# Performance work log

Measured on AMD Instinct MI355X. Metric: run time of the kernel, lower is better.

The kernel has to match this reference:

```python
import jax, jax.numpy as jnp
import numpy as np

B, C, T = 8, 512, 1024
EXP = 2
E = EXP * C          # 1024, gate/value width
H, HD = 8, 64        # heads, qk head dim
QK = H * HD          # 512
AVG_LEN = 512
EPS = 1e-5


def setup_inputs() -> dict:
    key = jax.random.key(0)
    ks = jax.random.split(key, 10)
    s = 0.02
    return {
        "x": jax.random.normal(ks[0], (B, C, T), jnp.float32),
        "W_in": jax.random.normal(ks[1], (2 * E, C), jnp.float32) * s,
        "b_in": jnp.zeros((2 * E,), jnp.float32),
        "W_attn": jax.random.normal(ks[2], (QK, C), jnp.float32) * s,
        "b_attn": jnp.zeros((QK,), jnp.float32),
        "w_q": 1.0 + jax.random.normal(ks[3], (QK,), jnp.float32) * 0.1,
        "b_q": jax.random.normal(ks[4], (QK,), jnp.float32) * 0.1,
        "w_k": 1.0 + jax.random.normal(ks[5], (QK,), jnp.float32) * 0.1,
        "b_k": jax.random.normal(ks[6], (QK,), jnp.float32) * 0.1,
        "W_out": jax.random.normal(ks[7], (C, E), jnp.float32) * s,
        "b_out": jnp.zeros((C,), jnp.float32),
        "gamma": jnp.ones((C,), jnp.float32),
    }


def reference(x, W_in, b_in, W_attn, b_attn, w_q, b_q, w_k, b_k, W_out, b_out, gamma):
    residual = x
    # mlp_in (1x1 conv) + SiLU, then chunk into gate u and value v, each (B,E,T)
    uv = jax.nn.silu(jnp.einsum('oc,bct->bot', W_in, x) + b_in[:, None])
    u, v = uv[:, :E], uv[:, E:]
    # mlp_attn (1x1 conv); no activation (activation_attn unused in forward)
    z = jnp.einsum('oc,bct->bot', W_attn, x) + b_attn[:, None]  # (B,QK,T)
    # depthwise 1x1 conv on cat(z,z) = two independent per-channel affines
    q = z * w_q[:, None] + b_q[:, None]
    k = z * w_k[:, None] + b_k[:, None]
    # split heads: q,k -> (B,H,T,HD); v -> (B,H,T,E//H)
    q = q.reshape(B, H, HD, T).transpose(0, 1, 3, 2)
    k = k.reshape(B, H, HD, T).transpose(0, 1, 3, 2)
    vh = v.reshape(B, H, E // H, T).transpose(0, 1, 3, 2)
    # entropy-invariant scale: (log n / log avg_len) / sqrt(d)
    scale = (np.log(T) / np.log(AVG_LEN)) / np.sqrt(HD)
    scores = jnp.einsum('bhqd,bhkd->bhqk', q, k) * jnp.float32(scale)
    attn = jax.nn.softmax(scores, axis=-1)
    o = jnp.einsum('bhqk,bhke->bhqe', attn, vh)        # (B,H,T,E//H)
    o = o.transpose(0, 1, 3, 2).reshape(B, E, T)       # back to (B,E,T)
    # gate, project out, residual + RMSNorm over channel dim
    out = jnp.einsum('ce,bet->bct', W_out, u * o) + b_out[:, None]
    y = residual + out
    rms = jax.lax.rsqrt(jnp.mean(y * y, axis=1, keepdims=True) + EPS)
    return y * rms * gamma[:, None]
```

## Files before the change

kernel.cpp:

```cpp
#include <hip/hip_runtime.h>

typedef __attribute__((ext_vector_type(8))) short short8;
typedef __attribute__((ext_vector_type(4))) float f32x4;
typedef __attribute__((ext_vector_type(16))) float f32x16;

__device__ __forceinline__ unsigned short f2b(float f) {
  union { float f; unsigned u; } x; x.f = f;
  unsigned r = (x.u + 0x7fffu + ((x.u >> 16) & 1u)) >> 16;
  return (unsigned short)r;
}
__device__ __forceinline__ float b2f(unsigned short b) {
  union { unsigned u; float f; } x; x.u = ((unsigned)b) << 16;
  return x.f;
}
__device__ __forceinline__ unsigned cvtpk(float lo, float hi) {
  unsigned r;
  asm("v_cvt_pk_bf16_f32 %0, %1, %2" : "=v"(r) : "v"(lo), "v"(hi));
  return r;
}
__device__ __forceinline__ void plswap(unsigned& a, unsigned& b) {
  asm volatile("v_permlane32_swap_b32 %0, %1" : "+v"(a), "+v"(b));
}

#define GLDS16(gp, lp)                                                                  \
  __builtin_amdgcn_global_load_lds((const __attribute__((address_space(1))) void*)(gp), \
                                   (__attribute__((address_space(3))) void*)(lp), 16, 0, 0)

__global__ void prep_w_kernel(const float* __restrict__ W_in, const float* __restrict__ W_attn,
                              const float* __restrict__ W_out, unsigned short* __restrict__ Wcat,
                              unsigned short* __restrict__ WoutB) {
  const int n1 = 2048 * 512, n2 = 512 * 512, n3 = 512 * 1024;
  for (int i = blockIdx.x * 256 + threadIdx.x; i < n1 + n2 + n3; i += gridDim.x * 256) {
    if (i < n1) Wcat[i] = f2b(W_in[i]);
    else if (i < n1 + n2) Wcat[i] = f2b(W_attn[i - n1]);
    else WoutB[i - n1 - n2] = f2b(W_out[i - n1 - n2]);
  }
}

__global__ __launch_bounds__(256) void transpose_x_kernel(const float* __restrict__ x,
                                                          unsigned short* __restrict__ xT) {
  __shared__ float tile[32][33];
  const int bid = blockIdx.x;
  const int b = bid >> 9;
  const int rem = bid & 511;
  const int c0 = (rem >> 5) << 5;
  const int t0 = (rem & 31) << 5;
  const int tj = threadIdx.x & 31, ti = threadIdx.x >> 5;
#pragma unroll
  for (int r = 0; r < 32; r += 8)
    tile[ti + r][tj] = x[(((size_t)b << 9) + c0 + ti + r) * 1024 + t0 + tj];
  __syncthreads();
#pragma unroll
  for (int r = 0; r < 32; r += 8)
    xT[(((size_t)b << 10) + t0 + ti + r) * 512 + c0 + tj] = f2b(tile[tj][ti + r]);
}

__device__ __forceinline__ void gemm_stage(const unsigned short* Ag, const unsigned short* Bg,
                                           int lda, int ldb, int k0, unsigned short* lsA,
                                           unsigned short* lsB, int buf, int sr, int sk,
                                           int ldst) {
  const int bb = buf * 8192;
  GLDS16(Ag + (size_t)sr * lda + k0 + sk, (char*)lsA + bb + ldst);
  GLDS16(Ag + (size_t)(sr + 64) * lda + k0 + sk, (char*)lsA + bb + 4096 + ldst);
  GLDS16(Bg + (size_t)sr * ldb + k0 + sk, (char*)lsB + bb + ldst);
  GLDS16(Bg + (size_t)(sr + 64) * ldb + k0 + sk, (char*)lsB + bb + 4096 + ldst);
}

__device__ __forceinline__ void gemm_bt_core(const unsigned short* __restrict__ Ag,
                                             const unsigned short* __restrict__ Bg, int lda,
                                             int ldb, int K, unsigned short* lsA,
                                             unsigned short* lsB, f32x4 acc[4][4]) {
  const int tid = threadIdx.x;
  const int lane = tid & 63;
  const int w = tid >> 6;
  const int wr = w >> 1, wc = w & 1;
  const int sr = tid >> 2;
  const int sk = (tid & 3) << 3;
  const int ldst = (tid >> 6) << 10;

  const int nt = K >> 5;
  gemm_stage(Ag, Bg, lda, ldb, 0, lsA, lsB, 0, sr, sk, ldst);
  for (int t = 0; t < nt; ++t) {
    const int cur = t & 1;
    if (t + 1 < nt) {
      gemm_stage(Ag, Bg, lda, ldb, (t + 1) << 5, lsA, lsB, cur ^ 1, sr, sk, ldst);
      asm volatile("s_waitcnt vmcnt(4)" ::: "memory");
    } else {
      asm volatile("s_waitcnt vmcnt(0)" ::: "memory");
    }
    __builtin_amdgcn_s_barrier();
    short8 af[4], bfr[4];
    const int bb = cur * 8192;
    const int ko = (lane >> 4) << 4;
    const int ra = (wr << 6) + (lane & 15);
    const int rb = (wc << 6) + (lane & 15);
#pragma unroll
    for (int mi = 0; mi < 4; ++mi)
      af[mi] = *(const short8*)((const char*)lsA + bb + ((ra + (mi << 4)) << 6) + ko);
#pragma unroll
    for (int ni = 0; ni < 4; ++ni)
      bfr[ni] = *(const short8*)((const char*)lsB + bb + ((rb + (ni << 4)) << 6) + ko);
#pragma unroll
    for (int mi = 0; mi < 4; ++mi)
#pragma unroll
      for (int ni = 0; ni < 4; ++ni)
        acc[mi][ni] =
            __builtin_amdgcn_mfma_f32_16x16x32_bf16(af[mi], bfr[ni], acc[mi][ni], 0, 0, 0);
    __builtin_amdgcn_s_barrier();
  }
}

__global__ __launch_bounds__(256) void gemm_a_kernel(
    const unsigned short* __restrict__ Wcat, const unsigned short* __restrict__ xT,
    const float* __restrict__ b_in, const float* __restrict__ b_attn,
    const float* __restrict__ w_q, const float* __restrict__ b_q, const float* __restrict__ w_k,
    const float* __restrict__ b_k, unsigned short* __restrict__ u, unsigned short* __restrict__ v,
    unsigned short* __restrict__ qT, unsigned short* __restrict__ kT) {
  __shared__ __align__(16) unsigned short lsA[8192];
  __shared__ __align__(16) unsigned short lsB[8192];
  const int bid = ((blockIdx.x & 7) * 160) + (blockIdx.x >> 3);
  const int b = bid / 160;
  const int rem = bid % 160;
  const int m0 = (rem >> 3) << 7;
  const int n0 = (rem & 7) << 7;
  f32x4 acc[4][4];
  const f32x4 z4 = {0.f, 0.f, 0.f, 0.f};
#pragma unroll
  for (int mi = 0; mi < 4; ++mi)
#pragma unroll
    for (int ni = 0; ni < 4; ++ni) acc[mi][ni] = z4;

  const unsigned short* Ag = Wcat + (size_t)m0 * 512;
  const unsigned short* Bg = xT + ((size_t)b << 19) + ((size_t)n0 << 9);
  gemm_bt_core(Ag, Bg, 512, 512, 512, lsA, lsB, acc);

  const int lane = threadIdx.x & 63;
  const int w = threadIdx.x >> 6;
  const int wr = w >> 1, wc = w & 1;
#pragma unroll
  for (int mi = 0; mi < 4; ++mi) {
    const int row0 = m0 + (wr << 6) + (mi << 4) + ((lane >> 4) << 2);
#pragma unroll
    for (int ni = 0; ni < 4; ++ni) {
      const int col = n0 + (wc << 6) + (ni << 4) + (lane & 15);
      if (row0 < 2048) {
#pragma unroll
        for (int i = 0; i < 4; ++i) {
          const int row = row0 + i;
          const float s = acc[mi][ni][i] + b_in[row];
          const float r = s / (1.f + __expf(-s));
          if (row < 1024)
            u[((((size_t)b << 10) + row) << 10) + col] = f2b(r);
          else
            v[((((size_t)b << 10) + (row - 1024)) << 10) + col] = f2b(r);
        }
      } else {
        const int c0 = row0 - 2048;
        ushort4 qv, kv;
        unsigned short* qp = (unsigned short*)&qv;
        unsigned short* kp = (unsigned short*)&kv;
#pragma unroll
        for (int i = 0; i < 4; ++i) {
          const int c = c0 + i;
          const float z = acc[mi][ni][i] + b_attn[c];
          qp[i] = f2b(z * w_q[c] + b_q[c]);
          kp[i] = f2b(z * w_k[c] + b_k[c]);
        }
        const int h = c0 >> 6, d = c0 & 63;
        const size_t base = ((((size_t)b * 8 + h) << 10) + col) * 64 + d;
        *(ushort4*)(qT + base) = qv;
        *(ushort4*)(kT + base) = kv;
      }
    }
  }
}

__global__ __launch_bounds__(256, 3) void attn_kernel(const unsigned short* __restrict__ qT,
                                                      const unsigned short* __restrict__ kT,
                                                      const unsigned short* __restrict__ v,
                                                      const unsigned short* __restrict__ u,
                                                      unsigned short* __restrict__ uoT) {
  __shared__ __align__(16) unsigned short Kls[2][4096];
  __shared__ __align__(16) unsigned short Vls[2][8192];
  __shared__ float lsumP[2][64];
  const float SCALE = 0.13888888888888889f;
  const int bid = blockIdx.x;
  const int bh = bid & 63;
  const int qb = bid >> 6;
  const int b = bh >> 3, h = bh & 7;
  const int tid = threadIdx.x;
  const int lane = tid & 63;
  const int w = tid >> 6;
  const int l5 = lane >> 5;
  const int l31 = lane & 31;
  const int qw = w >> 1, kw = w & 1;
  const int q0 = qb << 6;

  const unsigned short* qh = qT + ((size_t)bh << 16);
  const unsigned short* kh = kT + ((size_t)bh << 16);
  const unsigned short* vh = v + ((((size_t)b << 10) + (h << 7)) << 10);

  short8 qf[4];
#pragma unroll
  for (int ds = 0; ds < 4; ++ds)
    qf[ds] = *(const short8*)(qh + (size_t)(q0 + (qw << 5) + l31) * 64 + (ds << 4) + (l5 << 3));

  f32x16 o[4];
#pragma unroll
  for (int eb = 0; eb < 4; ++eb)
#pragma unroll
    for (int i = 0; i < 16; ++i) o[eb][i] = 0.f;
  float lacc = 0.f;

  const int srow = lane >> 3;
  const int scol = (((lane & 7) ^ srow) << 3);

#define ATTN_STAGE(buf, kt)                                                  \
  {                                                                          \
    const int t2 = (kt) << 6;                                                \
    _Pragma("unroll") for (int j = 0; j < 2; ++j)                            \
        GLDS16(kh + (size_t)(t2 + (w << 4) + (j << 3) + srow) * 64 + scol,   \
               (char*)Kls[buf] + (w << 11) + (j << 10));                     \
    _Pragma("unroll") for (int j = 0; j < 4; ++j)                            \
        GLDS16(vh + (size_t)((w << 5) + (j << 3) + srow) * 1024 + t2 + scol, \
               (char*)Vls[buf] + (w << 12) + (j << 10));                     \
  }

  ATTN_STAGE(0, 0);
  const int krow = (kw << 5) + l31;
  for (int kt = 0; kt < 16; ++kt) {
    const int cur = kt & 1;
    if (kt < 15) {
      ATTN_STAGE(cur ^ 1, kt + 1);
      asm volatile("s_waitcnt vmcnt(6)" ::: "memory");
    } else {
      asm volatile("s_waitcnt vmcnt(0)" ::: "memory");
    }
    __builtin_amdgcn_s_barrier();

    f32x16 s;
#pragma unroll
    for (int i = 0; i < 16; ++i) s[i] = 0.f;
    const char* kbase = (const char*)Kls[cur];
#pragma unroll
    for (int ds = 0; ds < 4; ++ds) {
      short8 kf = *(const short8*)(kbase + (krow << 7) +
                                   (((ds << 5) + (l5 << 4)) ^ ((krow & 7) << 4)));
      s = __builtin_amdgcn_mfma_f32_32x32x16_bf16(kf, qf[ds], s, 0, 0, 0);
    }
    float p[16];
#pragma unroll
    for (int i = 0; i < 16; ++i) {
      p[i] = __expf(s[i] * SCALE);
      lacc += p[i];
    }
    unsigned W00 = cvtpk(p[0], p[1]), W01 = cvtpk(p[2], p[3]);
    unsigned W10 = cvtpk(p[4], p[5]), W11 = cvtpk(p[6], p[7]);
    unsigned W20 = cvtpk(p[8], p[9]), W21 = cvtpk(p[10], p[11]);
    unsigned W30 = cvtpk(p[12], p[13]), W31 = cvtpk(p[14], p[15]);
    union { short8 s8; unsigned u4[4]; } pf0, pf1;
    {
      unsigned a = W10, bq = W00; plswap(a, bq);
      pf0.u4[0] = bq; pf0.u4[2] = a;
      unsigned c = W11, d = W01; plswap(c, d);
      pf0.u4[1] = d; pf0.u4[3] = c;
      unsigned e = W30, f = W20; plswap(e, f);
      pf1.u4[0] = f; pf1.u4[2] = e;
      unsigned g = W31, hh = W21; plswap(g, hh);
      pf1.u4[1] = hh; pf1.u4[3] = g;
    }

    const char* vbase = (const char*)Vls[cur];
#pragma unroll
    for (int eb = 0; eb < 4; ++eb) {
      const int vrow = (eb << 5) + l31;
      short8 vf0 = *(const short8*)(vbase + (vrow << 7) +
                                    ((((kw << 6)) + (l5 << 4)) ^ ((vrow & 7) << 4)));
      o[eb] = __builtin_amdgcn_mfma_f32_32x32x16_bf16(vf0, pf0.s8, o[eb], 0, 0, 0);
      short8 vf1 = *(const short8*)(vbase + (vrow << 7) +
                                    ((((kw << 6) + 32) + (l5 << 4)) ^ ((vrow & 7) << 4)));
      o[eb] = __builtin_amdgcn_mfma_f32_32x32x16_bf16(vf1, pf1.s8, o[eb], 0, 0, 0);
    }
    __builtin_amdgcn_s_barrier();
  }
#undef ATTN_STAGE

  lacc += __shfl_xor(lacc, 32, 64);
  if (l5 == 0) lsumP[kw][(qw << 5) + l31] = lacc;
  __syncthreads();

  float* red = (float*)Vls;
  if (kw == 1) {
#pragma unroll
    for (int eb = 0; eb < 4; ++eb)
#pragma unroll
      for (int i = 0; i < 16; ++i)
        red[((((qw << 2) + eb) << 10)) + (i << 6) + lane] = o[eb][i];
  }
  __syncthreads();

  if (kw == 0) {
    const int q = (qw << 5) + l31;
    const float rl = 1.f / (lsumP[0][q] + lsumP[1][q]);
    const int t = q0 + q;
#pragma unroll
    for (int eb = 0; eb < 4; ++eb) {
#pragma unroll
      for (int a = 0; a < 4; ++a) {
        const int e4 = (eb << 5) + (a << 3) + (l5 << 2);
        const int eg = (h << 7) + e4;
        ushort4 outv;
        unsigned short* op = (unsigned short*)&outv;
#pragma unroll
        for (int j = 0; j < 4; ++j) {
          const int i = (a << 2) + j;
          const float oo =
              (o[eb][i] + red[((((qw << 2) + eb) << 10)) + (i << 6) + lane]) * rl;
          const float uu = b2f(u[((((size_t)b << 10) + eg + j) << 10) + t]);
          op[j] = f2b(oo * uu);
        }
        *(ushort4*)(uoT + ((((size_t)b << 10) + t) << 10) + eg) = outv;
      }
    }
  }
}

__global__ __launch_bounds__(256) void gemm_c_kernel(const unsigned short* __restrict__ uoT,
                                                     const unsigned short* __restrict__ WoutB,
                                                     const float* __restrict__ x,
                                                     const float* __restrict__ b_out,
                                                     float* __restrict__ y) {
  __shared__ __align__(16) unsigned short lsA[8192];
  __shared__ __align__(16) unsigned short lsB[8192];
  const int bid = ((blockIdx.x & 7) * 32) + (blockIdx.x >> 3);
  const int b = bid >> 5;
  const int rem = bid & 31;
  const int m0 = (rem >> 2) << 7;
  const int n0 = (rem & 3) << 7;
  f32x4 acc[4][4];
  const f32x4 z4 = {0.f, 0.f, 0.f, 0.f};
#pragma unroll
  for (int mi = 0; mi < 4; ++mi)
#pragma unroll
    for (int ni = 0; ni < 4; ++ni) acc[mi][ni] = z4;

  const unsigned short* Ag = uoT + ((size_t)b << 20) + ((size_t)m0 << 10);
  const unsigned short* Bg = WoutB + ((size_t)n0 << 10);
  gemm_bt_core(Ag, Bg, 1024, 1024, 1024, lsA, lsB, acc);

  const int lane = threadIdx.x & 63;
  const int w = threadIdx.x >> 6;
  const int wr = w >> 1, wc = w & 1;
#pragma unroll
  for (int mi = 0; mi < 4; ++mi) {
    const int t4 = m0 + (wr << 6) + (mi << 4) + ((lane >> 4) << 2);
#pragma unroll
    for (int ni = 0; ni < 4; ++ni) {
      const int c = n0 + (wc << 6) + (ni << 4) + (lane & 15);
      const size_t base = ((((size_t)b << 9) + c) << 10) + t4;
      const f32x4 xv = *(const f32x4*)(x + base);
      const float bo = b_out[c];
      f32x4 o;
#pragma unroll
      for (int i = 0; i < 4; ++i) o[i] = acc[mi][ni][i] + bo + xv[i];
      *(f32x4*)(y + base) = o;
    }
  }
}

__global__ __launch_bounds__(256) void rms_kernel(const float* __restrict__ y,
                                                  const float* __restrict__ gamma,
                                                  float* __restrict__ out) {
  __shared__ float part[16][16];
  __shared__ float rmsv[16];
  const int bid = blockIdx.x;
  const int b = bid >> 6;
  const int t0 = (bid & 63) << 4;
  const int tid = threadIdx.x;
  const int tc = tid & 15, cg = tid >> 4;
  const int t = t0 + tc;
  float ss = 0.f;
  for (int c = cg * 32; c < cg * 32 + 32; ++c) {
    const float vv = y[((((size_t)b << 9) + c) << 10) + t];
    ss += vv * vv;
  }
  part[cg][tc] = ss;
  __syncthreads();
  if (tid < 16) {
    float tot = 0.f;
#pragma unroll
    for (int g = 0; g < 16; ++g) tot += part[g][tid];
    rmsv[tid] = rsqrtf(tot / 512.f + 1e-5f);
  }
  __syncthreads();
  const float rm = rmsv[tc];
  for (int c = cg * 32; c < cg * 32 + 32; ++c) {
    const size_t o = ((((size_t)b << 9) + c) << 10) + t;
    out[o] = y[o] * rm * gamma[c];
  }
}

extern "C" void kernel_launch(void* const* d_in, const int* in_sizes, int n_in, void* d_out,
                              int out_size, void* d_ws, size_t ws_size, hipStream_t stream) {
  const float* x = (const float*)d_in[0];
  const float* W_in = (const float*)d_in[1];
  const float* b_in = (const float*)d_in[2];
  const float* W_attn = (const float*)d_in[3];
  const float* b_attn = (const float*)d_in[4];
  const float* w_q = (const float*)d_in[5];
  const float* b_q = (const float*)d_in[6];
  const float* w_k = (const float*)d_in[7];
  const float* b_k = (const float*)d_in[8];
  const float* W_out = (const float*)d_in[9];
  const float* b_out = (const float*)d_in[10];
  const float* gamma = (const float*)d_in[11];
  float* out = (float*)d_out;

  char* ws = (char*)d_ws;
  size_t off = 0;
  auto alloc = [&](size_t bytes) {
    char* p = ws + off;
    off += (bytes + 255) & ~(size_t)255;
    return p;
  };
  unsigned short* Wcat = (unsigned short*)alloc((size_t)2560 * 512 * 2);
  unsigned short* WoutB = (unsigned short*)alloc((size_t)512 * 1024 * 2);
  unsigned short* xT = (unsigned short*)alloc((size_t)8 * 1024 * 512 * 2);
  unsigned short* u = (unsigned short*)alloc((size_t)8 * 1024 * 1024 * 2);
  unsigned short* v = (unsigned short*)alloc((size_t)8 * 1024 * 1024 * 2);
  unsigned short* qT = (unsigned short*)alloc((size_t)8 * 8 * 1024 * 64 * 2);
  unsigned short* kT = (unsigned short*)alloc((size_t)8 * 8 * 1024 * 64 * 2);
  unsigned short* uoT = (unsigned short*)alloc((size_t)8 * 1024 * 1024 * 2);
  float* y = (float*)alloc((size_t)8 * 512 * 1024 * 4);
  if (off > ws_size) return;

  prep_w_kernel<<<896, 256, 0, stream>>>(W_in, W_attn, W_out, Wcat, WoutB);
  transpose_x_kernel<<<4096, 256, 0, stream>>>(x, xT);
  gemm_a_kernel<<<1280, 256, 0, stream>>>(Wcat, xT, b_in, b_attn, w_q, b_q, w_k, b_k, u, v, qT,
                                          kT);
  attn_kernel<<<1024, 256, 0, stream>>>(qT, kT, v, u, uoT);
  gemm_c_kernel<<<256, 256, 0, stream>>>(uoT, WoutB, x, b_out, y);
  rms_kernel<<<512, 256, 0, stream>>>(y, gamma, out);
}
```

Measured before the change: 141.9 us.

## Restructure attention to split value columns per wave, remove cross-wave reduction

The attention kernel now uses 512-thread blocks over 128 queries. Each wave computes all 64 keys of a tile for its 32 queries and accumulates half of the 128 value columns, so the shared-memory reduction of partial outputs and row sums is no longer needed. It also adds XCD-aware block mapping and s_setprio around the MFMA sections. Separately, the RMS kernel keeps y values in registers to avoid re-reading them, and the GEMM kernels double their static LDS arrays, which may lower occupancy.

```diff
diff --git a/kernel.cpp b/kernel.cpp
--- a/kernel.cpp
+++ b/kernel.cpp
@@ -116,8 +116,8 @@
     const float* __restrict__ w_q, const float* __restrict__ b_q, const float* __restrict__ w_k,
     const float* __restrict__ b_k, unsigned short* __restrict__ u, unsigned short* __restrict__ v,
     unsigned short* __restrict__ qT, unsigned short* __restrict__ kT) {
-  __shared__ __align__(16) unsigned short lsA[8192];
-  __shared__ __align__(16) unsigned short lsB[8192];
+  __shared__ __align__(16) unsigned short lsA[16384];
+  __shared__ __align__(16) unsigned short lsB[16384];
   const int bid = ((blockIdx.x & 7) * 160) + (blockIdx.x >> 3);
   const int b = bid / 160;
   const int rem = bid % 160;
@@ -175,26 +175,26 @@
   }
 }
 
-__global__ __launch_bounds__(256, 3) void attn_kernel(const unsigned short* __restrict__ qT,
+__global__ __launch_bounds__(512, 4) void attn_kernel(const unsigned short* __restrict__ qT,
                                                       const unsigned short* __restrict__ kT,
                                                       const unsigned short* __restrict__ v,
                                                       const unsigned short* __restrict__ u,
                                                       unsigned short* __restrict__ uoT) {
   __shared__ __align__(16) unsigned short Kls[2][4096];
   __shared__ __align__(16) unsigned short Vls[2][8192];
-  __shared__ float lsumP[2][64];
   const float SCALE = 0.13888888888888889f;
-  const int bid = blockIdx.x;
-  const int bh = bid & 63;
-  const int qb = bid >> 6;
+  const int bx = blockIdx.x;
+  const int xcd = bx & 7, idx = bx >> 3;
+  const int bh = (xcd << 3) + (idx & 7);
+  const int qb = idx >> 3;
   const int b = bh >> 3, h = bh & 7;
   const int tid = threadIdx.x;
   const int lane = tid & 63;
   const int w = tid >> 6;
   const int l5 = lane >> 5;
   const int l31 = lane & 31;
-  const int qw = w >> 1, kw = w & 1;
-  const int q0 = qb << 6;
+  const int qw = w >> 1, eh = w & 1;
+  const int q0 = qb << 7;
 
   const unsigned short* qh = qT + ((size_t)bh << 16);
   const unsigned short* kh = kT + ((size_t)bh << 16);
@@ -205,122 +205,142 @@
   for (int ds = 0; ds < 4; ++ds)
     qf[ds] = *(const short8*)(qh + (size_t)(q0 + (qw << 5) + l31) * 64 + (ds << 4) + (l5 << 3));
 
-  f32x16 o[4];
-#pragma unroll
-  for (int eb = 0; eb < 4; ++eb)
+  f32x16 o[2];
+#pragma unroll
+  for (int eb = 0; eb < 2; ++eb)
 #pragma unroll
     for (int i = 0; i < 16; ++i) o[eb][i] = 0.f;
   float lacc = 0.f;
 
-  const int srow = lane >> 3;
-  const int scol = (((lane & 7) ^ srow) << 3);
-
-#define ATTN_STAGE(buf, kt)                                                  \
-  {                                                                          \
-    const int t2 = (kt) << 6;                                                \
-    _Pragma("unroll") for (int j = 0; j < 2; ++j)                            \
-        GLDS16(kh + (size_t)(t2 + (w << 4) + (j << 3) + srow) * 64 + scol,   \
-               (char*)Kls[buf] + (w << 11) + (j << 10));                     \
-    _Pragma("unroll") for (int j = 0; j < 4; ++j)                            \
-        GLDS16(vh + (size_t)((w << 5) + (j << 3) + srow) * 1024 + t2 + scol, \
-               (char*)Vls[buf] + (w << 12) + (j << 10));                     \
+  const int srow = tid >> 3;
+  const int scol = (((tid & 7) ^ (srow & 7)) << 3);
+
+#define ATTN_STAGE(buf, kt)                                                        \
+  {                                                                                \
+    const int t2 = (kt) << 6;                                                      \
+    GLDS16(kh + (size_t)(t2 + srow) * 64 + scol, (char*)Kls[buf] + (w << 10));     \
+    GLDS16(vh + ((size_t)srow << 10) + t2 + scol, (char*)Vls[buf] + (w << 10));    \
+    GLDS16(vh + ((size_t)(64 + srow) << 10) + t2 + scol,                           \
+           (char*)Vls[buf] + 8192 + (w << 10));                                    \
   }
 
   ATTN_STAGE(0, 0);
-  const int krow = (kw << 5) + l31;
+  union U8 { short8 s8; unsigned u4[4]; };
   for (int kt = 0; kt < 16; ++kt) {
     const int cur = kt & 1;
     if (kt < 15) {
       ATTN_STAGE(cur ^ 1, kt + 1);
-      asm volatile("s_waitcnt vmcnt(6)" ::: "memory");
+      asm volatile("s_waitcnt vmcnt(3)" ::: "memory");
     } else {
       asm volatile("s_waitcnt vmcnt(0)" ::: "memory");
     }
     __builtin_amdgcn_s_barrier();
 
-    f32x16 s;
-#pragma unroll
-    for (int i = 0; i < 16; ++i) s[i] = 0.f;
-    const char* kbase = (const char*)Kls[cur];
-#pragma unroll
-    for (int ds = 0; ds < 4; ++ds) {
-      short8 kf = *(const short8*)(kbase + (krow << 7) +
-                                   (((ds << 5) + (l5 << 4)) ^ ((krow & 7) << 4)));
-      s = __builtin_amdgcn_mfma_f32_32x32x16_bf16(kf, qf[ds], s, 0, 0, 0);
-    }
-    float p[16];
-#pragma unroll
-    for (int i = 0; i < 16; ++i) {
-      p[i] = __expf(s[i] * SCALE);
-      lacc += p[i];
-    }
-    unsigned W00 = cvtpk(p[0], p[1]), W01 = cvtpk(p[2], p[3]);
-    unsigned W10 = cvtpk(p[4], p[5]), W11 = cvtpk(p[6], p[7]);
-    unsigned W20 = cvtpk(p[8], p[9]), W21 = cvtpk(p[10], p[11]);
-    unsigned W30 = cvtpk(p[12], p[13]), W31 = cvtpk(p[14], p[15]);
-    union { short8 s8; unsigned u4[4]; } pf0, pf1;
+    const char* kb = (const char*)Kls[cur];
+    const char* vb = (const char*)Vls[cur];
+    U8 pf[4];
+
     {
+      f32x16 s;
+#pragma unroll
+      for (int i = 0; i < 16; ++i) s[i] = 0.f;
+      const int kr = l31;
+      __builtin_amdgcn_s_setprio(1);
+#pragma unroll
+      for (int ds = 0; ds < 4; ++ds) {
+        short8 kf = *(const short8*)(kb + (kr << 7) +
+                                     (((ds << 5) + (l5 << 4)) ^ ((kr & 7) << 4)));
+        s = __builtin_amdgcn_mfma_f32_32x32x16_bf16(kf, qf[ds], s, 0, 0, 0);
+      }
+      __builtin_amdgcn_s_setprio(0);
+      float p[16];
+#pragma unroll
+      for (int i = 0; i < 16; ++i) {
+        p[i] = __expf(s[i] * SCALE);
+        lacc += p[i];
+      }
+      unsigned W00 = cvtpk(p[0], p[1]), W01 = cvtpk(p[2], p[3]);
+      unsigned W10 = cvtpk(p[4], p[5]), W11 = cvtpk(p[6], p[7]);
+      unsigned W20 = cvtpk(p[8], p[9]), W21 = cvtpk(p[10], p[11]);
+      unsigned W30 = cvtpk(p[12], p[13]), W31 = cvtpk(p[14], p[15]);
       unsigned a = W10, bq = W00; plswap(a, bq);
-      pf0.u4[0] = bq; pf0.u4[2] = a;
+      pf[0].u4[0] = bq; pf[0].u4[2] = a;
       unsigned c = W11, d = W01; plswap(c, d);
-      pf0.u4[1] = d; pf0.u4[3] = c;
+      pf[0].u4[1] = d; pf[0].u4[3] = c;
       unsigned e = W30, f = W20; plswap(e, f);
-      pf1.u4[0] = f; pf1.u4[2] = e;
+      pf[1].u4[0] = f; pf[1].u4[2] = e;
       unsigned g = W31, hh = W21; plswap(g, hh);
-      pf1.u4[1] = hh; pf1.u4[3] = g;
-    }
-
-    const char* vbase = (const char*)Vls[cur];
-#pragma unroll
-    for (int eb = 0; eb < 4; ++eb) {
-      const int vrow = (eb << 5) + l31;
-      short8 vf0 = *(const short8*)(vbase + (vrow << 7) +
-                                    ((((kw << 6)) + (l5 << 4)) ^ ((vrow & 7) << 4)));
-      o[eb] = __builtin_amdgcn_mfma_f32_32x32x16_bf16(vf0, pf0.s8, o[eb], 0, 0, 0);
-      short8 vf1 = *(const short8*)(vbase + (vrow << 7) +
-                                    ((((kw << 6) + 32) + (l5 << 4)) ^ ((vrow & 7) << 4)));
-      o[eb] = __builtin_amdgcn_mfma_f32_32x32x16_bf16(vf1, pf1.s8, o[eb], 0, 0, 0);
-    }
+      pf[1].u4[1] = hh; pf[1].u4[3] = g;
+    }
+    {
+      f32x16 s;
+#pragma unroll
+      for (int i = 0; i < 16; ++i) s[i] = 0.f;
+      const int kr = 32 + l31;
+      __builtin_amdgcn_s_setprio(1);
+#pragma unroll
+      for (int ds = 0; ds < 4; ++ds) {
+        short8 kf = *(const short8*)(kb + (kr << 7) +
+                                     (((ds << 5) + (l5 << 4)) ^ ((kr & 7) << 4)));
+        s = __builtin_amdgcn_mfma_f32_32x32x16_bf16(kf, qf[ds], s, 0, 0, 0);
+      }
+      __builtin_amdgcn_s_setprio(0);
+      float p[16];
+#pragma unroll
+      for (int i = 0; i < 16; ++i) {
+        p[i] = __expf(s[i] * SCALE);
+        lacc += p[i];
+      }
+      unsigned W00 = cvtpk(p[0], p[1]), W01 = cvtpk(p[2], p[3]);
+      unsigned W10 = cvtpk(p[4], p[5]), W11 = cvtpk(p[6], p[7]);
+      unsigned W20 = cvtpk(p[8], p[9]), W21 = cvtpk(p[10], p[11]);
+      unsigned W30 = cvtpk(p[12], p[13]), W31 = cvtpk(p[14], p[15]);
+      unsigned a = W10, bq = W00; plswap(a, bq);
+      pf[2].u4[0] = bq; pf[2].u4[2] = a;
+      unsigned c = W11, d = W01; plswap(c, d);
+      pf[2].u4[1] = d; pf[2].u4[3] = c;
+      unsigned e = W30, f = W20; plswap(e, f);
+      pf[3].u4[0] = f; pf[3].u4[2] = e;
+      unsigned g = W31, hh = W21; plswap(g, hh);
+      pf[3].u4[1] = hh; pf[3].u4[3] = g;
+    }
+
+    __builtin_amdgcn_s_setprio(1);
+#pragma unroll
+    for (int eb = 0; eb < 2; ++eb) {
+      const int vrow = (eh << 6) + (eb << 5) + l31;
+#pragma unroll
+      for (int ks = 0; ks < 4; ++ks) {
+        short8 vf = *(const short8*)(vb + (vrow << 7) +
+                                     (((ks << 5) + (l5 << 4)) ^ ((vrow & 7) << 4)));
+        o[eb] = __builtin_amdgcn_mfma_f32_32x32x16_bf16(vf, pf[ks].s8, o[eb], 0, 0, 0);
+      }
+    }
+    __builtin_amdgcn_s_setprio(0);
     __builtin_amdgcn_s_barrier();
   }
 #undef ATTN_STAGE
 
   lacc += __shfl_xor(lacc, 32, 64);
-  if (l5 == 0) lsumP[kw][(qw << 5) + l31] = lacc;
-  __syncthreads();
-
-  float* red = (float*)Vls;
-  if (kw == 1) {
-#pragma unroll
-    for (int eb = 0; eb < 4; ++eb)
-#pragma unroll
-      for (int i = 0; i < 16; ++i)
-        red[((((qw << 2) + eb) << 10)) + (i << 6) + lane] = o[eb][i];
-  }
-  __syncthreads();
-
-  if (kw == 0) {
-    const int q = (qw << 5) + l31;
-    const float rl = 1.f / (lsumP[0][q] + lsumP[1][q]);
-    const int t = q0 + q;
-#pragma unroll
-    for (int eb = 0; eb < 4; ++eb) {
-#pragma unroll
-      for (int a = 0; a < 4; ++a) {
-        const int e4 = (eb << 5) + (a << 3) + (l5 << 2);
-        const int eg = (h << 7) + e4;
-        ushort4 outv;
-        unsigned short* op = (unsigned short*)&outv;
-#pragma unroll
-        for (int j = 0; j < 4; ++j) {
-          const int i = (a << 2) + j;
-          const float oo =
-              (o[eb][i] + red[((((qw << 2) + eb) << 10)) + (i << 6) + lane]) * rl;
-          const float uu = b2f(u[((((size_t)b << 10) + eg + j) << 10) + t]);
-          op[j] = f2b(oo * uu);
-        }
-        *(ushort4*)(uoT + ((((size_t)b << 10) + t) << 10) + eg) = outv;
-      }
+  const float rl = 1.f / lacc;
+  const int t = q0 + (qw << 5) + l31;
+
+#pragma unroll
+  for (int eb = 0; eb < 2; ++eb) {
+#pragma unroll
+    for (int a = 0; a < 4; ++a) {
+      const int e4 = (eh << 6) + (eb << 5) + (a << 3) + (l5 << 2);
+      const int eg = (h << 7) + e4;
+      ushort4 outv;
+      unsigned short* op = (unsigned short*)&outv;
+#pragma unroll
+      for (int j = 0; j < 4; ++j) {
+        const int i = (a << 2) + j;
+        const float oo = o[eb][i] * rl;
+        const float uu = b2f(u[((((size_t)b << 10) + eg + j) << 10) + t]);
+        op[j] = f2b(oo * uu);
+      }
+      *(ushort4*)(uoT + ((((size_t)b << 10) + t) << 10) + eg) = outv;
     }
   }
 }
@@ -330,8 +350,8 @@
                                                      const float* __restrict__ x,
                                                      const float* __restrict__ b_out,
                                                      float* __restrict__ y) {
-  __shared__ __align__(16) unsigned short lsA[8192];
-  __shared__ __align__(16) unsigned short lsB[8192];
+  __shared__ __align__(16) unsigned short lsA[16384];
+  __shared__ __align__(16) unsigned short lsB[16384];
   const int bid = ((blockIdx.x & 7) * 32) + (blockIdx.x >> 3);
   const int b = bid >> 5;
   const int rem = bid & 31;
@@ -371,32 +391,37 @@
 __global__ __launch_bounds__(256) void rms_kernel(const float* __restrict__ y,
                                                   const float* __restrict__ gamma,
                                                   float* __restrict__ out) {
-  __shared__ float part[16][16];
-  __shared__ float rmsv[16];
+  __shared__ float part[8][32];
+  __shared__ float rmsv[32];
   const int bid = blockIdx.x;
-  const int b = bid >> 6;
-  const int t0 = (bid & 63) << 4;
+  const int b = bid >> 5;
+  const int t0 = (bid & 31) << 5;
   const int tid = threadIdx.x;
-  const int tc = tid & 15, cg = tid >> 4;
-  const int t = t0 + tc;
+  const int tt = tid & 31, cg = tid >> 5;
+  const int t = t0 + tt;
+  float vals[64];
   float ss = 0.f;
-  for (int c = cg * 32; c < cg * 32 + 32; ++c) {
+#pragma unroll
+  for (int ci = 0; ci < 64; ++ci) {
+    const int c = (cg << 6) + ci;
     const float vv = y[((((size_t)b << 9) + c) << 10) + t];
+    vals[ci] = vv;
     ss += vv * vv;
   }
-  part[cg][tc] = ss;
+  part[cg][tt] = ss;
   __syncthreads();
-  if (tid < 16) {
+  if (tid < 32) {
     float tot = 0.f;
 #pragma unroll
-    for (int g = 0; g < 16; ++g) tot += part[g][tid];
+    for (int g = 0; g < 8; ++g) tot += part[g][tid];
     rmsv[tid] = rsqrtf(tot / 512.f + 1e-5f);
   }
   __syncthreads();
-  const float rm = rmsv[tc];
-  for (int c = cg * 32; c < cg * 32 + 32; ++c) {
-    const size_t o = ((((size_t)b << 9) + c) << 10) + t;
-    out[o] = y[o] * rm * gamma[c];
+  const float rm = rmsv[tt];
+#pragma unroll
+  for (int ci = 0; ci < 64; ++ci) {
+    const int c = (cg << 6) + ci;
+    out[((((size_t)b << 9) + c) << 10) + t] = vals[ci] * rm * gamma[c];
   }
 }
 
@@ -438,7 +463,7 @@
   transpose_x_kernel<<<4096, 256, 0, stream>>>(x, xT);
   gemm_a_kernel<<<1280, 256, 0, stream>>>(Wcat, xT, b_in, b_attn, w_q, b_q, w_k, b_k, u, v, qT,
                                           kT);
-  attn_kernel<<<1024, 256, 0, stream>>>(qT, kT, v, u, uoT);
+  attn_kernel<<<512, 512, 0, stream>>>(qT, kT, v, u, uoT);
   gemm_c_kernel<<<256, 256, 0, stream>>>(uoT, WoutB, x, b_out, y);
-  rms_kernel<<<512, 256, 0, stream>>>(y, gamma, out);
-}
+  rms_kernel<<<256, 256, 0, stream>>>(y, gamma, out);
+}
```

Result: slower. 145.4 us (+2.5%).
